# Performance work log

Measured on AMD Instinct MI355X. Metric: run time of the kernel, lower is better.

## Reference

```python
import jax, jax.numpy as jnp
import numpy as np

BIT_DEPTH = 8  # feature squeezing

def setup_inputs() -> dict:
    key = jax.random.key(0)
    ks = jax.random.split(key, 8)
    B, C, H, W = 8, 256, 64, 64
    Cq = C // 8
    x = jax.random.normal(ks[0], (B, C, H, W), dtype=jnp.float32)
    # 1x1 conv weights stored as [out, in] (kernel dims squeezed)
    wq = jax.random.normal(ks[1], (Cq, C), dtype=jnp.float32) * 0.05
    bq = jax.random.normal(ks[2], (Cq,), dtype=jnp.float32) * 0.05
    wk = jax.random.normal(ks[3], (Cq, C), dtype=jnp.float32) * 0.05
    bk = jax.random.normal(ks[4], (Cq,), dtype=jnp.float32) * 0.05
    wv = jax.random.normal(ks[5], (C, C), dtype=jnp.float32) * 0.05
    bv = jax.random.normal(ks[6], (C,), dtype=jnp.float32) * 0.05
    gamma = jax.random.normal(ks[7], (1,), dtype=jnp.float32) * 0.1
    return {"x": x, "wq": wq, "bq": bq, "wk": wk, "bk": bk, "wv": wv, "bv": bv, "gamma": gamma}

def reference(x, wq, bq, wk, bk, wv, bv, gamma):
    B, C, H, W = x.shape
    N = H * W
    xf = x.reshape(B, C, N)  # flatten spatial
    # 1x1 convs == per-pixel linear projections
    q = jnp.einsum('bcn,oc->bon', xf, wq) + bq[None, :, None]   # [B, C/8, N]
    k = jnp.einsum('bcn,oc->bon', xf, wk) + bk[None, :, None]   # [B, C/8, N]
    v = jnp.einsum('bcn,oc->bon', xf, wv) + bv[None, :, None]   # [B, C, N]
    energy = jnp.einsum('bcn,bcm->bnm', q, k)                   # [B, N, N] (no scaling, as in source)
    attn = jax.nn.softmax(energy, axis=-1)
    out = jnp.einsum('bcm,bnm->bcn', v, attn).reshape(B, C, H, W)
    out = gamma[0] * out + out               # gamma-scaled residual of attention output
    scale = jnp.float32(2 ** BIT_DEPTH)
    return jnp.floor(out * scale) / scale    # feature squeezing (bit_depth=8)
```

## Files before the change

kernel.cpp:

```cpp
#include <hip/hip_runtime.h>
#include <math.h>

namespace {
constexpr int BB = 8;
constexpr int CH = 256;
constexpr int NN = 4096;
}

typedef float f32x4 __attribute__((ext_vector_type(4)));
typedef short bf16x8 __attribute__((ext_vector_type(8)));
typedef unsigned short us8 __attribute__((ext_vector_type(8)));

#define MFMA16(a, b, c) __builtin_amdgcn_mfma_f32_16x16x32_bf16(a, b, c, 0, 0, 0)

__device__ __forceinline__ unsigned short f2bf(float x) {
    unsigned int u = __float_as_uint(x);
    u += 0x7fffu + ((u >> 16) & 1u);
    return (unsigned short)(u >> 16);
}
__device__ __forceinline__ float bf2f(unsigned short h) {
    return __uint_as_float(((unsigned int)h) << 16);
}

__global__ __launch_bounds__(256) void wsplit_kernel(
    const float* __restrict__ wq, const float* __restrict__ wk,
    const float* __restrict__ wv,
    unsigned short* __restrict__ wh, unsigned short* __restrict__ wl)
{
    int idx = blockIdx.x * 256 + threadIdx.x;
    float v;
    if (idx < 8192)       v = wq[idx];
    else if (idx < 16384) v = wk[idx - 8192];
    else                  v = wv[idx - 16384];
    unsigned short hi = f2bf(v);
    wh[idx] = hi;
    wl[idx] = f2bf(v - bf2f(hi));
}

#define PJ_XH 0
#define PJ_XL 32768
#define PJ_VE 0
#define PJ_QK 36864

__global__ __launch_bounds__(256, 2) void proj_kernel(
    const float* __restrict__ x,
    const unsigned short* __restrict__ wh, const unsigned short* __restrict__ wl,
    const float* __restrict__ bq, const float* __restrict__ bk,
    const float* __restrict__ bv,
    unsigned short* __restrict__ qh, unsigned short* __restrict__ ql,
    unsigned short* __restrict__ kh, unsigned short* __restrict__ kl,
    unsigned short* __restrict__ vt)
{
    __shared__ __align__(16) unsigned char smem[65536];
    const int t    = threadIdx.x;
    const int lane = t & 63;
    const int w    = t >> 6;
    const int l16  = lane & 15;
    const int quad = lane >> 4;
    const int b    = blockIdx.x >> 6;
    const int n0   = (blockIdx.x & 63) << 6;

    const int cc = t & 15, pg = t >> 4;
    const float* xg = x + (size_t)b * 256 * NN + n0 + pg * 4;
    float4 xv[16];
    #pragma unroll
    for (int jc = 0; jc < 16; ++jc)
        xv[jc] = *(const float4*)(xg + (size_t)(jc * 16 + cc) * NN);
    #pragma unroll
    for (int jc = 0; jc < 16; ++jc) {
        const int c = jc * 16 + cc;
        const int chunkb = c >> 3, cb = (c & 7) * 2;
        #pragma unroll
        for (int p = 0; p < 4; ++p) {
            const int n = pg * 4 + p;
            float v = (p == 0) ? xv[jc].x : (p == 1) ? xv[jc].y
                    : (p == 2) ? xv[jc].z : xv[jc].w;
            unsigned short hi = f2bf(v);
            unsigned short lo = f2bf(v - bf2f(hi));
            int off = n * 512 + ((chunkb ^ (n & 7)) * 16) + cb;
            *(unsigned short*)(smem + PJ_XH + off) = hi;
            *(unsigned short*)(smem + PJ_XL + off) = lo;
        }
    }
    __syncthreads();

    f32x4 acc[5][4] = {};
    #pragma unroll 1
    for (int kc = 0; kc < 8; ++kc) {
        bf16x8 ah[5], al[5];
        #pragma unroll
        for (int i = 0; i < 5; ++i) {
            int och = (w * 5 + i) * 16 + l16;
            ah[i] = *(const bf16x8*)(wh + och * 256 + kc * 32 + quad * 8);
            al[i] = *(const bf16x8*)(wl + och * 256 + kc * 32 + quad * 8);
        }
        #pragma unroll
        for (int nt = 0; nt < 4; ++nt) {
            int roff = (nt * 16 + l16) * 512 + (((kc * 4 + quad) ^ (l16 & 7)) * 16);
            bf16x8 bh = *(const bf16x8*)(smem + PJ_XH + roff);
            bf16x8 bl = *(const bf16x8*)(smem + PJ_XL + roff);
            #pragma unroll
            for (int i = 0; i < 5; ++i) {
                acc[i][nt] = MFMA16(ah[i], bh, acc[i][nt]);
                acc[i][nt] = MFMA16(al[i], bh, acc[i][nt]);
                acc[i][nt] = MFMA16(ah[i], bl, acc[i][nt]);
            }
        }
    }
    __syncthreads();

    #pragma unroll
    for (int i = 0; i < 5; ++i) {
        int tile = w * 5 + i;
        if (tile < 4) {
            #pragma unroll
            for (int r = 0; r < 4; ++r) {
                int och = tile * 16 + quad * 4 + r;
                float bias = (och < 32) ? bq[och] : bk[och - 32];
                int arr = (och < 32) ? 0 : 2;
                int oq = och & 31;
                #pragma unroll
                for (int nt = 0; nt < 4; ++nt) {
                    float val = acc[i][nt][r] + bias;
                    unsigned short hi = f2bf(val);
                    unsigned short lo = f2bf(val - bf2f(hi));
                    *(unsigned short*)(smem + PJ_QK + arr * 4096 + (nt * 16 + l16) * 64 + oq * 2) = hi;
                    *(unsigned short*)(smem + PJ_QK + (arr + 1) * 4096 + (nt * 16 + l16) * 64 + oq * 2) = lo;
                }
            }
        } else {
            #pragma unroll
            for (int r = 0; r < 4; ++r) {
                int voch = tile * 16 + quad * 4 + r - 64;
                float bias = bv[voch];
                #pragma unroll
                for (int nt = 0; nt < 4; ++nt) {
                    *(unsigned short*)(smem + PJ_VE + voch * 136 + (nt * 16 + l16) * 2)
                        = f2bf(acc[i][nt][r] + bias);
                }
            }
        }
    }
    __syncthreads();

    {
        unsigned short* dsts[4] = { qh, ql, kh, kl };
        int arr = t >> 6, rn = t & 63;
        unsigned short* dst = dsts[arr] + ((size_t)b * NN + n0 + rn) * 32;
        #pragma unroll
        for (int i = 0; i < 4; ++i)
            *(us8*)(dst + i * 8) = *(const us8*)(smem + PJ_QK + arr * 4096 + rn * 64 + i * 16);
    }
    #pragma unroll
    for (int p = 0; p < 4; ++p) {
        int voch = p * 64 + (t >> 2), piece = t & 3;
        unsigned short* dst = vt + ((size_t)b * CH + voch) * NN + n0 + piece * 16;
        *(us8*)(dst)     = *(const us8*)(smem + PJ_VE + voch * 136 + piece * 32);
        *(us8*)(dst + 8) = *(const us8*)(smem + PJ_VE + voch * 136 + piece * 32 + 16);
    }
}

#define AP_PAD 144
#define AS_OFF 18432

__global__ __launch_bounds__(256, 2) void attn_kernel(
    const unsigned short* __restrict__ qh, const unsigned short* __restrict__ ql,
    const unsigned short* __restrict__ kh, const unsigned short* __restrict__ kl,
    const unsigned short* __restrict__ vt, const float* __restrict__ gptr,
    float* __restrict__ out)
{
    __shared__ __align__(16) unsigned char smem[19456];
    const int t    = threadIdx.x;
    const int lane = t & 63;
    const int w    = t >> 6;
    const int l16  = lane & 15;
    const int quad = lane >> 4;
    const int b    = blockIdx.x & 7;
    const int n0   = (blockIdx.x >> 3) << 6;

    bf16x8 qhA[4], qlA[4];
    #pragma unroll
    for (int qt = 0; qt < 4; ++qt) {
        size_t row = (size_t)b * NN + n0 + qt * 16 + l16;
        qhA[qt] = *(const bf16x8*)(qh + row * 32 + quad * 8);
        qlA[qt] = *(const bf16x8*)(ql + row * 32 + quad * 8);
    }

    const unsigned char* kp  = (const unsigned char*)kh
        + ((size_t)b * NN + w * 16 + l16) * 64 + quad * 16;
    const unsigned char* klp = (const unsigned char*)kl
        + ((size_t)b * NN + w * 16 + l16) * 64 + quad * 16;
    const unsigned char* vp  = (const unsigned char*)vt
        + ((size_t)b * CH + w * 64 + l16) * (NN * 2) + quad * 16;

    bf16x8 kfh[2], kfl[2], vf[2][8];
    kfh[0] = *(const bf16x8*)kp;
    kfl[0] = *(const bf16x8*)klp;

    f32x4 acc[4][4] = {};
    float S[4][4] = {};

    #pragma unroll 2
    for (int r = 0; r < 64; ++r) {
        if (r < 63) {
            kfh[(r + 1) & 1] = *(const bf16x8*)(kp  + (size_t)(r + 1) * 4096);
            kfl[(r + 1) & 1] = *(const bf16x8*)(klp + (size_t)(r + 1) * 4096);
        }
        #pragma unroll
        for (int ct = 0; ct < 4; ++ct)
            #pragma unroll
            for (int ks = 0; ks < 2; ++ks)
                vf[r & 1][ct * 2 + ks] = *(const bf16x8*)
                    (vp + (size_t)ct * 131072 + ks * 64 + (size_t)r * 128);

        {
            unsigned char* pb = smem + (r & 1) * 9216;
            const bf16x8 bh = kfh[r & 1], bl = kfl[r & 1];
            #pragma unroll
            for (int qt = 0; qt < 4; ++qt) {
                f32x4 e = { 0.f, 0.f, 0.f, 0.f };
                e = MFMA16(qhA[qt], bh, e);
                e = MFMA16(qlA[qt], bh, e);
                e = MFMA16(qhA[qt], bl, e);
                #pragma unroll
                for (int rr = 0; rr < 4; ++rr) {
                    float p = __expf(e[rr]);
                    unsigned short pv16 = f2bf(p);
                    S[qt][rr] += bf2f(pv16);
                    *(unsigned short*)(pb + (qt * 16 + quad * 4 + rr) * AP_PAD
                                          + (w * 16 + l16) * 2) = pv16;
                }
            }
        }
        if (r > 0) {
            const unsigned char* pp = smem + ((r - 1) & 1) * 9216;
            #pragma unroll
            for (int ks = 0; ks < 2; ++ks) {
                bf16x8 aP[4];
                #pragma unroll
                for (int qt = 0; qt < 4; ++qt)
                    aP[qt] = *(const bf16x8*)(pp + (qt * 16 + l16) * AP_PAD
                                                 + ks * 64 + quad * 16);
                #pragma unroll
                for (int qt = 0; qt < 4; ++qt)
                    #pragma unroll
                    for (int ct = 0; ct < 4; ++ct)
                        acc[qt][ct] = MFMA16(aP[qt], vf[(r - 1) & 1][ct * 2 + ks],
                                             acc[qt][ct]);
            }
        }
        __syncthreads();
    }
    {
        const unsigned char* pp = smem + 9216;
        #pragma unroll
        for (int ks = 0; ks < 2; ++ks) {
            bf16x8 aP[4];
            #pragma unroll
            for (int qt = 0; qt < 4; ++qt)
                aP[qt] = *(const bf16x8*)(pp + (qt * 16 + l16) * AP_PAD
                                             + ks * 64 + quad * 16);
            #pragma unroll
            for (int qt = 0; qt < 4; ++qt)
                #pragma unroll
                for (int ct = 0; ct < 4; ++ct)
                    acc[qt][ct] = MFMA16(aP[qt], vf[1][ct * 2 + ks], acc[qt][ct]);
        }
    }

    #pragma unroll
    for (int mask = 1; mask <= 8; mask <<= 1)
        #pragma unroll
        for (int qt = 0; qt < 4; ++qt)
            #pragma unroll
            for (int rr = 0; rr < 4; ++rr)
                S[qt][rr] += __shfl_xor(S[qt][rr], mask);
    float* SM = (float*)(smem + AS_OFF);
    if (l16 == 0) {
        #pragma unroll
        for (int qt = 0; qt < 4; ++qt)
            #pragma unroll
            for (int rr = 0; rr < 4; ++rr)
                SM[w * 64 + qt * 16 + quad * 4 + rr] = S[qt][rr];
    }
    __syncthreads();

    const float g1 = 1.f + gptr[0];
    float* ob = out + (size_t)b * CH * NN;
    #pragma unroll
    for (int qt = 0; qt < 4; ++qt) {
        float is[4];
        #pragma unroll
        for (int rr = 0; rr < 4; ++rr) {
            int qi = qt * 16 + quad * 4 + rr;
            float Sf = SM[qi] + SM[64 + qi] + SM[128 + qi] + SM[192 + qi];
            is[rr] = g1 / Sf;
        }
        #pragma unroll
        for (int ct = 0; ct < 4; ++ct) {
            float4 o4;
            o4.x = floorf(acc[qt][ct][0] * is[0] * 256.f) * 0.00390625f;
            o4.y = floorf(acc[qt][ct][1] * is[1] * 256.f) * 0.00390625f;
            o4.z = floorf(acc[qt][ct][2] * is[2] * 256.f) * 0.00390625f;
            o4.w = floorf(acc[qt][ct][3] * is[3] * 256.f) * 0.00390625f;
            *(float4*)(ob + (size_t)(w * 64 + ct * 16 + l16) * NN
                          + n0 + qt * 16 + quad * 4) = o4;
        }
    }
}

extern "C" void kernel_launch(void* const* d_in, const int* in_sizes, int n_in,
                              void* d_out, int out_size, void* d_ws, size_t ws_size,
                              hipStream_t stream) {
    const float* x  = (const float*)d_in[0];
    const float* wq = (const float*)d_in[1];
    const float* bq = (const float*)d_in[2];
    const float* wk = (const float*)d_in[3];
    const float* bk = (const float*)d_in[4];
    const float* wv = (const float*)d_in[5];
    const float* bv = (const float*)d_in[6];
    const float* gm = (const float*)d_in[7];
    float* out = (float*)d_out;

    unsigned short* ws = (unsigned short*)d_ws;
    const size_t WSZ = 320 * 256;
    const size_t QSZ = (size_t)BB * NN * 32;
    unsigned short* wh = ws;
    unsigned short* wl = wh + WSZ;
    unsigned short* qh = wl + WSZ;
    unsigned short* ql = qh + QSZ;
    unsigned short* kh = ql + QSZ;
    unsigned short* kl = kh + QSZ;
    unsigned short* vt = kl + QSZ;

    wsplit_kernel<<<320, 256, 0, stream>>>(wq, wk, wv, wh, wl);
    proj_kernel<<<512, 256, 0, stream>>>(x, wh, wl, bq, bk, bv,
                                         qh, ql, kh, kl, vt);
    attn_kernel<<<512, 256, 0, stream>>>(qh, ql, kh, kl, vt, gm, out);
}
```

Before: 254.0 us.

## Restructure attention to keep P in registers and stage V via LDS DMA

The attention kernel is reorganized so that each wave owns 32 queries and 128 channels and computes the transposed energy tile, K·Q. This lets the exponentiated probabilities be packed straight into MFMA B-operands in registers instead of round-tripping through shared memory. V tiles are now double-buffered into a 64KB LDS region with global_load_lds (with XOR swizzle), and the V layout from the projection kernel is permuted to match the new P register layout. The projection kernel also packs pairs of bf16 values into 32-bit LDS stores and prefetches weight fragments one k-step ahead. The larger LDS footprint may reduce occupancy, and each wave now recomputes QK for all 64 keys, which duplicates energy MFMAs across channel groups.

After: 303.2 us. 19.4% more time.

```diff
diff --git a/kernel.cpp b/kernel.cpp
--- a/kernel.cpp
+++ b/kernel.cpp
@@ -10,6 +10,7 @@
 typedef float f32x4 __attribute__((ext_vector_type(4)));
 typedef short bf16x8 __attribute__((ext_vector_type(8)));
 typedef unsigned short us8 __attribute__((ext_vector_type(8)));
+typedef unsigned int u32x4 __attribute__((ext_vector_type(4)));
 
 #define MFMA16(a, b, c) __builtin_amdgcn_mfma_f32_16x16x32_bf16(a, b, c, 0, 0, 0)
 
@@ -20,6 +21,14 @@
 }
 __device__ __forceinline__ float bf2f(unsigned short h) {
     return __uint_as_float(((unsigned int)h) << 16);
+}
+__device__ __forceinline__ void gload16(const void* g, void* l) {
+    __builtin_amdgcn_global_load_lds(
+        (const __attribute__((address_space(1))) unsigned int*)g,
+        (__attribute__((address_space(3))) unsigned int*)l, 16, 0, 0);
+}
+__device__ __forceinline__ float vget(const float4& v, int p) {
+    return (p == 0) ? v.x : (p == 1) ? v.y : (p == 2) ? v.z : v.w;
 }
 
 __global__ __launch_bounds__(256) void wsplit_kernel(
@@ -60,39 +69,50 @@
     const int b    = blockIdx.x >> 6;
     const int n0   = (blockIdx.x & 63) << 6;
 
-    const int cc = t & 15, pg = t >> 4;
-    const float* xg = x + (size_t)b * 256 * NN + n0 + pg * 4;
-    float4 xv[16];
-    #pragma unroll
-    for (int jc = 0; jc < 16; ++jc)
-        xv[jc] = *(const float4*)(xg + (size_t)(jc * 16 + cc) * NN);
-    #pragma unroll
-    for (int jc = 0; jc < 16; ++jc) {
-        const int c = jc * 16 + cc;
-        const int chunkb = c >> 3, cb = (c & 7) * 2;
+    const int cp   = t & 127;
+    const int half = t >> 7;
+    const float* xg = x + (size_t)b * 256 * NN + n0 + half * 32;
+    float4 xa[8], xb[8];
+    #pragma unroll
+    for (int i = 0; i < 8; ++i) {
+        xa[i] = *(const float4*)(xg + (size_t)(2 * cp) * NN + i * 4);
+        xb[i] = *(const float4*)(xg + (size_t)(2 * cp + 1) * NN + i * 4);
+    }
+    #pragma unroll
+    for (int i = 0; i < 8; ++i) {
         #pragma unroll
         for (int p = 0; p < 4; ++p) {
-            const int n = pg * 4 + p;
-            float v = (p == 0) ? xv[jc].x : (p == 1) ? xv[jc].y
-                    : (p == 2) ? xv[jc].z : xv[jc].w;
-            unsigned short hi = f2bf(v);
-            unsigned short lo = f2bf(v - bf2f(hi));
-            int off = n * 512 + ((chunkb ^ (n & 7)) * 16) + cb;
-            *(unsigned short*)(smem + PJ_XH + off) = hi;
-            *(unsigned short*)(smem + PJ_XL + off) = lo;
-        }
+            const int n = half * 32 + i * 4 + p;
+            float v0 = vget(xa[i], p), v1 = vget(xb[i], p);
+            unsigned int h0 = f2bf(v0), h1 = f2bf(v1);
+            unsigned int l0 = f2bf(v0 - bf2f((unsigned short)h0));
+            unsigned int l1 = f2bf(v1 - bf2f((unsigned short)h1));
+            const int chunk = (cp >> 2) ^ (n & 7);
+            const int off = n * 512 + chunk * 16 + (cp & 3) * 4;
+            *(unsigned int*)(smem + PJ_XH + off) = h0 | (h1 << 16);
+            *(unsigned int*)(smem + PJ_XL + off) = l0 | (l1 << 16);
+        }
+    }
+
+    bf16x8 ah[2][5], al[2][5];
+    #pragma unroll
+    for (int i = 0; i < 5; ++i) {
+        int och = (w * 5 + i) * 16 + l16;
+        ah[0][i] = *(const bf16x8*)(wh + och * 256 + quad * 8);
+        al[0][i] = *(const bf16x8*)(wl + och * 256 + quad * 8);
     }
     __syncthreads();
 
     f32x4 acc[5][4] = {};
-    #pragma unroll 1
+    #pragma unroll 2
     for (int kc = 0; kc < 8; ++kc) {
-        bf16x8 ah[5], al[5];
-        #pragma unroll
-        for (int i = 0; i < 5; ++i) {
-            int och = (w * 5 + i) * 16 + l16;
-            ah[i] = *(const bf16x8*)(wh + och * 256 + kc * 32 + quad * 8);
-            al[i] = *(const bf16x8*)(wl + och * 256 + kc * 32 + quad * 8);
+        if (kc < 7) {
+            #pragma unroll
+            for (int i = 0; i < 5; ++i) {
+                int och = (w * 5 + i) * 16 + l16;
+                ah[(kc + 1) & 1][i] = *(const bf16x8*)(wh + och * 256 + (kc + 1) * 32 + quad * 8);
+                al[(kc + 1) & 1][i] = *(const bf16x8*)(wl + och * 256 + (kc + 1) * 32 + quad * 8);
+            }
         }
         #pragma unroll
         for (int nt = 0; nt < 4; ++nt) {
@@ -101,9 +121,9 @@
             bf16x8 bl = *(const bf16x8*)(smem + PJ_XL + roff);
             #pragma unroll
             for (int i = 0; i < 5; ++i) {
-                acc[i][nt] = MFMA16(ah[i], bh, acc[i][nt]);
-                acc[i][nt] = MFMA16(al[i], bh, acc[i][nt]);
-                acc[i][nt] = MFMA16(ah[i], bl, acc[i][nt]);
+                acc[i][nt] = MFMA16(ah[kc & 1][i], bh, acc[i][nt]);
+                acc[i][nt] = MFMA16(al[kc & 1][i], bh, acc[i][nt]);
+                acc[i][nt] = MFMA16(ah[kc & 1][i], bl, acc[i][nt]);
             }
         }
     }
@@ -135,7 +155,9 @@
                 float bias = bv[voch];
                 #pragma unroll
                 for (int nt = 0; nt < 4; ++nt) {
-                    *(unsigned short*)(smem + PJ_VE + voch * 136 + (nt * 16 + l16) * 2)
+                    int col  = nt * 16 + l16;
+                    int pcol = (col & 32) | ((col & 12) << 1) | (col & 3) | ((col >> 2) & 4);
+                    *(unsigned short*)(smem + PJ_VE + voch * 136 + pcol * 2)
                         = f2bf(acc[i][nt][r] + bias);
                 }
             }
@@ -159,9 +181,6 @@
         *(us8*)(dst + 8) = *(const us8*)(smem + PJ_VE + voch * 136 + piece * 32 + 16);
     }
 }
-
-#define AP_PAD 144
-#define AS_OFF 18432
 
 __global__ __launch_bounds__(256, 2) void attn_kernel(
     const unsigned short* __restrict__ qh, const unsigned short* __restrict__ ql,
@@ -169,7 +188,7 @@
     const unsigned short* __restrict__ vt, const float* __restrict__ gptr,
     float* __restrict__ out)
 {
-    __shared__ __align__(16) unsigned char smem[19456];
+    __shared__ __align__(16) unsigned char smem[65536];
     const int t    = threadIdx.x;
     const int lane = t & 63;
     const int w    = t >> 6;
@@ -177,134 +196,117 @@
     const int quad = lane >> 4;
     const int b    = blockIdx.x & 7;
     const int n0   = (blockIdx.x >> 3) << 6;
-
-    bf16x8 qhA[4], qlA[4];
-    #pragma unroll
-    for (int qt = 0; qt < 4; ++qt) {
-        size_t row = (size_t)b * NN + n0 + qt * 16 + l16;
-        qhA[qt] = *(const bf16x8*)(qh + row * 32 + quad * 8);
-        qlA[qt] = *(const bf16x8*)(ql + row * 32 + quad * 8);
-    }
-
-    const unsigned char* kp  = (const unsigned char*)kh
-        + ((size_t)b * NN + w * 16 + l16) * 64 + quad * 16;
-    const unsigned char* klp = (const unsigned char*)kl
-        + ((size_t)b * NN + w * 16 + l16) * 64 + quad * 16;
-    const unsigned char* vp  = (const unsigned char*)vt
-        + ((size_t)b * CH + w * 64 + l16) * (NN * 2) + quad * 16;
-
-    bf16x8 kfh[2], kfl[2], vf[2][8];
-    kfh[0] = *(const bf16x8*)kp;
-    kfl[0] = *(const bf16x8*)klp;
-
-    f32x4 acc[4][4] = {};
-    float S[4][4] = {};
+    const int qgrp = w & 1;
+    const int cgrp = w >> 1;
+
+    bf16x8 qB[2][2];
+    #pragma unroll
+    for (int qt = 0; qt < 2; ++qt) {
+        size_t row = (size_t)b * NN + n0 + qgrp * 32 + qt * 16 + l16;
+        qB[qt][0] = *(const bf16x8*)(qh + row * 32 + quad * 8);
+        qB[qt][1] = *(const bf16x8*)(ql + row * 32 + quad * 8);
+    }
+
+    const unsigned char* khb = (const unsigned char*)(kh + (size_t)b * NN * 32);
+    const unsigned char* klb = (const unsigned char*)(kl + (size_t)b * NN * 32);
+    const int vr = t >> 3, vc = t & 7;
+    const unsigned char* vsrc0 = (const unsigned char*)vt
+        + (size_t)b * CH * NN * 2 + (size_t)vr * 8192 + (vc ^ (vr & 7)) * 16;
+
+    #pragma unroll
+    for (int j = 0; j < 8; ++j)
+        gload16(vsrc0 + (size_t)j * 262144, smem + (j * 256 + t) * 16);
+    bf16x8 khf[2][4], klf[2][4];
+    #pragma unroll
+    for (int kt = 0; kt < 4; ++kt) {
+        khf[0][kt] = *(const bf16x8*)(khb + (kt * 16 + l16) * 64 + quad * 16);
+        klf[0][kt] = *(const bf16x8*)(klb + (kt * 16 + l16) * 64 + quad * 16);
+    }
+    __syncthreads();
+
+    f32x4 acc[8][2] = {};
+    float S[2] = {};
+    unsigned int pk[2][4][2];
 
     #pragma unroll 2
     for (int r = 0; r < 64; ++r) {
+        const int cur = r & 1, nxt = (r + 1) & 1;
         if (r < 63) {
-            kfh[(r + 1) & 1] = *(const bf16x8*)(kp  + (size_t)(r + 1) * 4096);
-            kfl[(r + 1) & 1] = *(const bf16x8*)(klp + (size_t)(r + 1) * 4096);
-        }
-        #pragma unroll
-        for (int ct = 0; ct < 4; ++ct)
-            #pragma unroll
-            for (int ks = 0; ks < 2; ++ks)
-                vf[r & 1][ct * 2 + ks] = *(const bf16x8*)
-                    (vp + (size_t)ct * 131072 + ks * 64 + (size_t)r * 128);
-
-        {
-            unsigned char* pb = smem + (r & 1) * 9216;
-            const bf16x8 bh = kfh[r & 1], bl = kfl[r & 1];
-            #pragma unroll
-            for (int qt = 0; qt < 4; ++qt) {
+            #pragma unroll
+            for (int j = 0; j < 8; ++j)
+                gload16(vsrc0 + (size_t)j * 262144 + (size_t)(r + 1) * 128,
+                        smem + nxt * 32768 + (j * 256 + t) * 16);
+        }
+        #pragma unroll
+        for (int kt = 0; kt < 4; ++kt) {
+            #pragma unroll
+            for (int qt = 0; qt < 2; ++qt) {
                 f32x4 e = { 0.f, 0.f, 0.f, 0.f };
-                e = MFMA16(qhA[qt], bh, e);
-                e = MFMA16(qlA[qt], bh, e);
-                e = MFMA16(qhA[qt], bl, e);
+                e = MFMA16(khf[cur][kt], qB[qt][0], e);
+                e = MFMA16(khf[cur][kt], qB[qt][1], e);
+                e = MFMA16(klf[cur][kt], qB[qt][0], e);
+                unsigned int pb[4];
                 #pragma unroll
                 for (int rr = 0; rr < 4; ++rr) {
                     float p = __expf(e[rr]);
-                    unsigned short pv16 = f2bf(p);
-                    S[qt][rr] += bf2f(pv16);
-                    *(unsigned short*)(pb + (qt * 16 + quad * 4 + rr) * AP_PAD
-                                          + (w * 16 + l16) * 2) = pv16;
+                    pb[rr] = f2bf(p);
+                    S[qt] += bf2f((unsigned short)pb[rr]);
                 }
-            }
-        }
-        if (r > 0) {
-            const unsigned char* pp = smem + ((r - 1) & 1) * 9216;
-            #pragma unroll
-            for (int ks = 0; ks < 2; ++ks) {
-                bf16x8 aP[4];
-                #pragma unroll
-                for (int qt = 0; qt < 4; ++qt)
-                    aP[qt] = *(const bf16x8*)(pp + (qt * 16 + l16) * AP_PAD
-                                                 + ks * 64 + quad * 16);
-                #pragma unroll
-                for (int qt = 0; qt < 4; ++qt)
-                    #pragma unroll
-                    for (int ct = 0; ct < 4; ++ct)
-                        acc[qt][ct] = MFMA16(aP[qt], vf[(r - 1) & 1][ct * 2 + ks],
-                                             acc[qt][ct]);
+                pk[qt][kt][0] = pb[0] | (pb[1] << 16);
+                pk[qt][kt][1] = pb[2] | (pb[3] << 16);
+            }
+        }
+        if (r < 63) {
+            #pragma unroll
+            for (int kt = 0; kt < 4; ++kt) {
+                size_t off = (size_t)((r + 1) * 64 + kt * 16 + l16) * 64 + quad * 16;
+                khf[nxt][kt] = *(const bf16x8*)(khb + off);
+                klf[nxt][kt] = *(const bf16x8*)(klb + off);
+            }
+        }
+        const unsigned char* vb = smem + cur * 32768;
+        #pragma unroll
+        for (int s = 0; s < 2; ++s) {
+            union { u32x4 u; bf16x8 v; } pf[2];
+            #pragma unroll
+            for (int qt = 0; qt < 2; ++qt) {
+                pf[qt].u[0] = pk[qt][2 * s][0];
+                pf[qt].u[1] = pk[qt][2 * s][1];
+                pf[qt].u[2] = pk[qt][2 * s + 1][0];
+                pf[qt].u[3] = pk[qt][2 * s + 1][1];
+            }
+            #pragma unroll
+            for (int ct = 0; ct < 8; ++ct) {
+                int row = cgrp * 128 + ct * 16 + l16;
+                bf16x8 vf = *(const bf16x8*)
+                    (vb + row * 128 + (((s * 4 + quad) ^ (l16 & 7)) * 16));
+                acc[ct][0] = MFMA16(vf, pf[0].v, acc[ct][0]);
+                acc[ct][1] = MFMA16(vf, pf[1].v, acc[ct][1]);
             }
         }
         __syncthreads();
     }
-    {
-        const unsigned char* pp = smem + 9216;
-        #pragma unroll
-        for (int ks = 0; ks < 2; ++ks) {
-            bf16x8 aP[4];
-            #pragma unroll
-            for (int qt = 0; qt < 4; ++qt)
-                aP[qt] = *(const bf16x8*)(pp + (qt * 16 + l16) * AP_PAD
-                                             + ks * 64 + quad * 16);
-            #pragma unroll
-            for (int qt = 0; qt < 4; ++qt)
-                #pragma unroll
-                for (int ct = 0; ct < 4; ++ct)
-                    acc[qt][ct] = MFMA16(aP[qt], vf[1][ct * 2 + ks], acc[qt][ct]);
-        }
-    }
-
-    #pragma unroll
-    for (int mask = 1; mask <= 8; mask <<= 1)
-        #pragma unroll
-        for (int qt = 0; qt < 4; ++qt)
-            #pragma unroll
-            for (int rr = 0; rr < 4; ++rr)
-                S[qt][rr] += __shfl_xor(S[qt][rr], mask);
-    float* SM = (float*)(smem + AS_OFF);
-    if (l16 == 0) {
-        #pragma unroll
-        for (int qt = 0; qt < 4; ++qt)
-            #pragma unroll
-            for (int rr = 0; rr < 4; ++rr)
-                SM[w * 64 + qt * 16 + quad * 4 + rr] = S[qt][rr];
-    }
-    __syncthreads();
-
+
+    #pragma unroll
+    for (int qt = 0; qt < 2; ++qt) {
+        S[qt] += __shfl_xor(S[qt], 16);
+        S[qt] += __shfl_xor(S[qt], 32);
+    }
     const float g1 = 1.f + gptr[0];
+    float is[2] = { g1 / S[0], g1 / S[1] };
+
     float* ob = out + (size_t)b * CH * NN;
     #pragma unroll
-    for (int qt = 0; qt < 4; ++qt) {
-        float is[4];
-        #pragma unroll
-        for (int rr = 0; rr < 4; ++rr) {
-            int qi = qt * 16 + quad * 4 + rr;
-            float Sf = SM[qi] + SM[64 + qi] + SM[128 + qi] + SM[192 + qi];
-            is[rr] = g1 / Sf;
-        }
-        #pragma unroll
-        for (int ct = 0; ct < 4; ++ct) {
-            float4 o4;
-            o4.x = floorf(acc[qt][ct][0] * is[0] * 256.f) * 0.00390625f;
-            o4.y = floorf(acc[qt][ct][1] * is[1] * 256.f) * 0.00390625f;
-            o4.z = floorf(acc[qt][ct][2] * is[2] * 256.f) * 0.00390625f;
-            o4.w = floorf(acc[qt][ct][3] * is[3] * 256.f) * 0.00390625f;
-            *(float4*)(ob + (size_t)(w * 64 + ct * 16 + l16) * NN
-                          + n0 + qt * 16 + quad * 4) = o4;
+    for (int ct = 0; ct < 8; ++ct) {
+        #pragma unroll
+        for (int qt = 0; qt < 2; ++qt) {
+            #pragma unroll
+            for (int rr = 0; rr < 4; ++rr) {
+                int ch = cgrp * 128 + ct * 16 + quad * 4 + rr;
+                int n  = n0 + qgrp * 32 + qt * 16 + l16;
+                float val = floorf(acc[ct][qt][rr] * is[qt] * 256.f) * 0.00390625f;
+                ob[(size_t)ch * NN + n] = val;
+            }
         }
     }
 }
```
